# Kernel optimization log

Measured on AMD Instinct MI355X. Metric: run time of the kernel, lower is better.

The kernel has to match this reference:

```python
import jax, jax.numpy as jnp
import numpy as np


def setup_inputs() -> dict:
    key = jax.random.key(0)
    ks = jax.random.split(key, 6)
    N, C, H = 3072, 2048, 16
    hd = C // H  # 128
    x = jax.random.normal(ks[0], (N, C), dtype=jnp.float32)
    # rotary frequencies as cos/sin of per-position angles (real view of complex freqs_cis)
    inv_freq = 1.0 / (10000.0 ** (np.arange(0, hd, 2, dtype=np.float32) / hd))  # [hd/2]
    angles = jnp.arange(N, dtype=jnp.float32)[:, None] * jnp.asarray(inv_freq)[None, :]  # [N, hd/2]
    freqs_cos = jnp.cos(angles)
    freqs_sin = jnp.sin(angles)
    qkv_w = jax.random.normal(ks[1], (3 * C, C), dtype=jnp.float32) * 0.02
    qkv_b = jnp.zeros((3 * C,), dtype=jnp.float32)
    proj_w = jax.random.normal(ks[2], (C, C), dtype=jnp.float32) * 0.02
    proj_b = jnp.zeros((C,), dtype=jnp.float32)
    cu_seqlens = jnp.array([0, 768, 1536, 2304, 3072], dtype=jnp.int32)
    return {
        "x": x, "freqs_cos": freqs_cos, "freqs_sin": freqs_sin,
        "qkv_w": qkv_w, "qkv_b": qkv_b, "proj_w": proj_w, "proj_b": proj_b,
        "cu_seqlens": cu_seqlens, "max_seqlen": 768,
    }


def _rope(t, cos, sin):
    # t: [H, N, hd]; interpret consecutive pairs as complex, multiply by freqs_cis
    tr, ti = t[..., 0::2], t[..., 1::2]              # [H, N, hd/2]
    o_re = tr * cos - ti * sin
    o_im = tr * sin + ti * cos
    return jnp.stack([o_re, o_im], axis=-1).reshape(t.shape)


def reference(x, freqs_cos, freqs_sin, qkv_w, qkv_b, proj_w, proj_b, cu_seqlens, max_seqlen):
    N, C = x.shape
    hd = freqs_cos.shape[-1] * 2
    H = C // hd
    qkv = (x @ qkv_w.T + qkv_b).reshape(N, 3, H, hd).transpose(1, 2, 0, 3)  # [3, H, N, hd]
    q, k, v = qkv[0], qkv[1], qkv[2]
    q = _rope(q, freqs_cos, freqs_sin)
    k = _rope(k, freqs_cos, freqs_sin)
    # varlen attention: block-diagonal mask from cu_seqlens segment membership
    seg = jnp.searchsorted(cu_seqlens[1:], jnp.arange(N), side="right")  # [N]
    mask = seg[:, None] == seg[None, :]                                  # [N, N]
    scale = 1.0 / np.sqrt(hd).astype(np.float32)
    scores = jnp.einsum("hnd,hmd->hnm", q, k) * scale                    # [H, N, N]
    scores = jnp.where(mask[None], scores, jnp.finfo(scores.dtype).min)
    probs = jax.nn.softmax(scores, axis=-1)
    out = jnp.einsum("hnm,hmd->hnd", probs, v)                           # [H, N, hd]
    out = out.transpose(1, 0, 2).reshape(N, C)
    return out @ proj_w.T + proj_b
```

## Files before the change

kernel.cpp:

```cpp
#include <hip/hip_runtime.h>
#include <stdint.h>

#define N_TOK  3072
#define C_DIM  2048
#define K3C    6144
#define NHEAD  16
#define HD     128
#define SEGLEN 768

typedef __attribute__((ext_vector_type(8))) short  short8;
typedef __attribute__((ext_vector_type(4))) float  f32x4;

__device__ __forceinline__ unsigned short f2bf(float f) {
  unsigned u = __builtin_bit_cast(unsigned, f);
  u += 0x7FFFu + ((u >> 16) & 1u);
  return (unsigned short)(u >> 16);
}
__device__ __forceinline__ float bf2f(unsigned short h) {
  unsigned u = ((unsigned)h) << 16;
  return __builtin_bit_cast(float, u);
}
__device__ __forceinline__ void gload_lds16(const void* g, void* l) {
  __builtin_amdgcn_global_load_lds(
      (const __attribute__((address_space(1))) unsigned int*)g,
      (__attribute__((address_space(3))) unsigned int*)l, 16, 0, 0);
}

#define XB_ELEMS    (3072L*2048L)
#define WQKV_ELEMS  (6144L*2048L)
#define WPROJ_ELEMS (2048L*2048L)
__global__ __launch_bounds__(256) void cast_bf16_kernel(
    const float* __restrict__ x, const float* __restrict__ wqkv,
    const float* __restrict__ wproj, unsigned short* __restrict__ xb,
    unsigned short* __restrict__ wqkvb, unsigned short* __restrict__ wprojb) {
  long t = (long)blockIdx.x * 256 + threadIdx.x;
  long i = t * 8;
  const float* src; unsigned short* dst; long off;
  if (i < XB_ELEMS)                   { src = x;     dst = xb;     off = i; }
  else if (i < XB_ELEMS + WQKV_ELEMS) { src = wqkv;  dst = wqkvb;  off = i - XB_ELEMS; }
  else                                { src = wproj; dst = wprojb; off = i - XB_ELEMS - WQKV_ELEMS; }
  f32x4 a = *(const f32x4*)(src + off);
  f32x4 b = *(const f32x4*)(src + off + 4);
  short8 o;
  #pragma unroll
  for (int k = 0; k < 4; ++k) { o[k] = (short)f2bf(a[k]); o[k+4] = (short)f2bf(b[k]); }
  *(short8*)(dst + off) = o;
}

template<bool OUTF32>
__global__ __launch_bounds__(256) void gemm_bt(
    const unsigned short* __restrict__ A, const unsigned short* __restrict__ B,
    const float* __restrict__ bias, void* __restrict__ Cout,
    int M, int N, int K) {
  __shared__ unsigned short sA[128*32];
  __shared__ unsigned short sB[128*32];
  const int tid = threadIdx.x;
  const int w  = tid >> 6, l = tid & 63;
  const int lr = l & 15,  lh = l >> 4;
  const int wr = w >> 1,  wc = w & 1;
  const long row0 = (long)blockIdx.y * 128;
  const long col0 = (long)blockIdx.x * 128;
  f32x4 acc[4][4] = {};

  const int c0 = w*128 + l;
  const int c1 = c0 + 64;
  const int r0 = c0 >> 2, k0 = (c0 & 3) * 8;
  const int r1 = c1 >> 2, k1 = (c1 & 3) * 8;

  for (int kt = 0; kt < K; kt += 32) {
    __syncthreads();
    gload_lds16(A + (row0 + r0)*K + kt + k0, (char*)sA + (size_t)(w*2+0)*1024);
    gload_lds16(A + (row0 + r1)*K + kt + k1, (char*)sA + (size_t)(w*2+1)*1024);
    gload_lds16(B + (col0 + r0)*K + kt + k0, (char*)sB + (size_t)(w*2+0)*1024);
    gload_lds16(B + (col0 + r1)*K + kt + k1, (char*)sB + (size_t)(w*2+1)*1024);
    __syncthreads();

    short8 af[4], bfr[4];
    #pragma unroll
    for (int m = 0; m < 4; ++m) af[m]  = *(const short8*)&sA[(wr*64 + m*16 + lr)*32 + lh*8];
    #pragma unroll
    for (int n = 0; n < 4; ++n) bfr[n] = *(const short8*)&sB[(wc*64 + n*16 + lr)*32 + lh*8];
    #pragma unroll
    for (int m = 0; m < 4; ++m)
      #pragma unroll
      for (int n = 0; n < 4; ++n)
        acc[m][n] = __builtin_amdgcn_mfma_f32_16x16x32_bf16(af[m], bfr[n], acc[m][n], 0, 0, 0);
  }

  #pragma unroll
  for (int n = 0; n < 4; ++n) {
    const long col = col0 + wc*64 + n*16 + lr;
    const float bv = bias[col];
    #pragma unroll
    for (int m = 0; m < 4; ++m) {
      const long rbase = row0 + wr*64 + m*16 + lh*4;
      #pragma unroll
      for (int r = 0; r < 4; ++r) {
        float val = acc[m][n][r] + bv;
        if constexpr (OUTF32) ((float*)Cout)[(rbase + r)*N + col] = val;
        else ((unsigned short*)Cout)[(rbase + r)*N + col] = f2bf(val);
      }
    }
  }
}

__global__ __launch_bounds__(256) void rope_kernel(
    unsigned short* __restrict__ qkv, const float* __restrict__ fcos,
    const float* __restrict__ fsin) {
  long t = (long)blockIdx.x * 256 + threadIdx.x;
  int n  = (int)(t >> 9);
  int col = (int)(t & 511) * 8;
  int j0 = (col & 127) >> 1;
  unsigned short* p = qkv + (long)n * K3C + col;
  short8 v = *(short8*)p;
  f32x4 vc = *(const f32x4*)(fcos + n*64 + j0);
  f32x4 vs = *(const f32x4*)(fsin + n*64 + j0);
  short8 o;
  #pragma unroll
  for (int i = 0; i < 4; ++i) {
    float re = bf2f((unsigned short)v[2*i]);
    float im = bf2f((unsigned short)v[2*i+1]);
    float c = vc[i], s = vs[i];
    o[2*i]   = (short)f2bf(re*c - im*s);
    o[2*i+1] = (short)f2bf(re*s + im*c);
  }
  *(short8*)p = o;
}

__global__ __launch_bounds__(256) void transpose_v_kernel(
    const unsigned short* __restrict__ qkv, unsigned short* __restrict__ vT) {
  __shared__ unsigned short sT[64*64];
  int bidx = blockIdx.x;
  const int nb = (bidx % 48) * 64; bidx /= 48;
  const int db = (bidx & 1) * 64;  bidx >>= 1;
  const int h  = bidx;
  const int tid = threadIdx.x;
  #pragma unroll
  for (int p = 0; p < 2; ++p) {
    int ch = tid + p*256;
    int row = ch >> 3, c8 = ch & 7;
    f32x4 val = *(const f32x4*)(qkv + (long)(nb + row)*K3C + 4096 + h*HD + db + c8*8);
    int off = (row*128 + c8*16) ^ ((row & 7) << 4);
    *(f32x4*)((char*)sT + off) = val;
  }
  __syncthreads();
  #pragma unroll
  for (int p = 0; p < 2; ++p) {
    int ch = tid + p*256;
    int drow = ch >> 3, nc = ch & 7;
    short8 tv;
    #pragma unroll
    for (int j = 0; j < 8; ++j) {
      int nn = nc*8 + j;
      int off = (nn*128 + drow*2) ^ ((nn & 7) << 4);
      tv[j] = *(const short*)((const char*)sT + off);
    }
    *(short8*)(vT + ((long)h*HD + db + drow)*N_TOK + nb + nc*8) = tv;
  }
}

__global__ __launch_bounds__(256) void attn_kernel(
    const unsigned short* __restrict__ qkv, const unsigned short* __restrict__ vT,
    unsigned short* __restrict__ attb) {
  __shared__ unsigned short sK [64*128];
  __shared__ unsigned short sVT[128*64];
  __shared__ unsigned short sP [4][16*72];
  const int tid = threadIdx.x;
  const int w = tid >> 6, l = tid & 63, lr = l & 15, lh = l >> 4;
  int bidx = blockIdx.x;
  const int qt = bidx % 12; bidx /= 12;
  const int h  = bidx & 15; bidx >>= 4;
  const int s  = bidx;
  const int n0 = s*SEGLEN + qt*64;
  const float scale = 0.08838834764831845f;
  const float LOG2E = 1.4426950408889634f;

  short8 aq[4];
  {
    const unsigned short* qrow = qkv + (long)(n0 + w*16 + lr)*K3C + h*HD;
    #pragma unroll
    for (int c = 0; c < 4; ++c) aq[c] = *(const short8*)(qrow + c*32 + lh*8);
  }
  f32x4 o[8] = {};
  float m_r[4] = {-1e30f, -1e30f, -1e30f, -1e30f};
  float l_r[4] = {0.f, 0.f, 0.f, 0.f};

  for (int kt = 0; kt < 12; ++kt) {
    const int kb = s*SEGLEN + kt*64;
    __syncthreads();
    #pragma unroll
    for (int p = 0; p < 4; ++p) {
      int ch = (p*4 + w)*64 + l;
      int key = ch >> 4;
      int kc  = (ch & 15) ^ (key & 7);
      gload_lds16(qkv + (long)(kb + key)*K3C + C_DIM + h*HD + kc*8,
                  (char*)sK + (size_t)(p*4 + w)*1024);
      int d   = ch >> 3;
      int kc2 = (ch & 7) ^ (d & 7);
      gload_lds16(vT + ((long)h*HD + d)*N_TOK + kb + kc2*8,
                  (char*)sVT + (size_t)(p*4 + w)*1024);
    }
    __syncthreads();

    f32x4 sacc[4] = {};
    #pragma unroll
    for (int kd = 0; kd < 4; ++kd)
      #pragma unroll
      for (int kf = 0; kf < 4; ++kf) {
        int key = kf*16 + lr;
        int off = (key*256 + kd*64 + lh*16) ^ ((key & 7) << 4);
        short8 bk = *(const short8*)((const char*)sK + off);
        sacc[kf] = __builtin_amdgcn_mfma_f32_16x16x32_bf16(aq[kd], bk, sacc[kf], 0, 0, 0);
      }

    float alpha[4];
    #pragma unroll
    for (int r = 0; r < 4; ++r) {
      float v0 = fmaxf(fmaxf(sacc[0][r], sacc[1][r]), fmaxf(sacc[2][r], sacc[3][r]));
      #pragma unroll
      for (int sh = 1; sh < 16; sh <<= 1) v0 = fmaxf(v0, __shfl_xor(v0, sh, 64));
      float pm = v0 * scale;
      float mn = fmaxf(m_r[r], pm);
      alpha[r] = __builtin_exp2f((m_r[r] - mn) * LOG2E);
      m_r[r] = mn;
    }
    float rsum[4] = {0.f, 0.f, 0.f, 0.f};
    #pragma unroll
    for (int kf = 0; kf < 4; ++kf)
      #pragma unroll
      for (int r = 0; r < 4; ++r) {
        float pv = __builtin_exp2f((sacc[kf][r]*scale - m_r[r]) * LOG2E);
        rsum[r] += pv;
        sP[w][(lh*4 + r)*72 + kf*16 + lr] = f2bf(pv);
      }
    #pragma unroll
    for (int r = 0; r < 4; ++r) {
      float t = rsum[r];
      #pragma unroll
      for (int sh = 1; sh < 16; sh <<= 1) t += __shfl_xor(t, sh, 64);
      l_r[r] = l_r[r]*alpha[r] + t;
    }
    #pragma unroll
    for (int nf = 0; nf < 8; ++nf)
      #pragma unroll
      for (int r = 0; r < 4; ++r) o[nf][r] *= alpha[r];

    #pragma unroll
    for (int ks = 0; ks < 2; ++ks) {
      short8 ap = *(const short8*)&sP[w][lr*72 + ks*32 + lh*8];
      #pragma unroll
      for (int nf = 0; nf < 8; ++nf) {
        int d = nf*16 + lr;
        int off = (d*128 + ks*64 + lh*16) ^ ((d & 7) << 4);
        short8 bv = *(const short8*)((const char*)sVT + off);
        o[nf] = __builtin_amdgcn_mfma_f32_16x16x32_bf16(ap, bv, o[nf], 0, 0, 0);
      }
    }
  }

  #pragma unroll
  for (int r = 0; r < 4; ++r) {
    float inv = 1.0f / l_r[r];
    int n = n0 + w*16 + lh*4 + r;
    unsigned short* orow = attb + (long)n*C_DIM + h*HD;
    #pragma unroll
    for (int nf = 0; nf < 8; ++nf) orow[nf*16 + lr] = f2bf(o[nf][r] * inv);
  }
}

extern "C" void kernel_launch(void* const* d_in, const int* in_sizes, int n_in,
                              void* d_out, int out_size, void* d_ws, size_t ws_size,
                              hipStream_t stream) {
  (void)in_sizes; (void)n_in; (void)out_size; (void)ws_size;
  const float* x      = (const float*)d_in[0];
  const float* fcos   = (const float*)d_in[1];
  const float* fsin   = (const float*)d_in[2];
  const float* qkv_w  = (const float*)d_in[3];
  const float* qkv_b  = (const float*)d_in[4];
  const float* proj_w = (const float*)d_in[5];
  const float* proj_b = (const float*)d_in[6];

  char* ws = (char*)d_ws;
  unsigned short* xb     = (unsigned short*)(ws + 0L);
  unsigned short* wqkvb  = (unsigned short*)(ws + 12582912L);
  unsigned short* wprojb = (unsigned short*)(ws + 37748736L);
  unsigned short* qkvb   = (unsigned short*)(ws + 46137344L);
  unsigned short* vT     = (unsigned short*)(ws + 83886080L);
  unsigned short* attb   = xb;

  cast_bf16_kernel<<<11264, 256, 0, stream>>>(x, qkv_w, proj_w, xb, wqkvb, wprojb);
  gemm_bt<false><<<dim3(48, 24), 256, 0, stream>>>(xb, wqkvb, qkv_b, qkvb, 3072, 6144, 2048);
  rope_kernel<<<6144, 256, 0, stream>>>(qkvb, fcos, fsin);
  transpose_v_kernel<<<1536, 256, 0, stream>>>(qkvb, vT);
  attn_kernel<<<768, 256, 0, stream>>>(qkvb, vT, attb);
  gemm_bt<true><<<dim3(16, 24), 256, 0, stream>>>(attb, wprojb, proj_b, d_out, 3072, 2048, 2048);
}
```

Before: 419.0 us.

## Replace GEMM with 256x256-tile 8-wave double-buffered pipelined kernel

Replaces the simple 128x128 single-buffered bf16 GEMM with a 512-thread kernel that computes 256x256 output tiles. Global-to-LDS loads are staged ahead into double buffers, with explicit vmcnt waits, barriers and setprio around MFMA bursts, so memory traffic overlaps compute. This raises data reuse per tile and hides load latency. In exchange it uses far more registers and LDS. The projection GEMM now launches only 96 blocks, which may underfill the GPU.

```diff
diff --git a/kernel.cpp b/kernel.cpp
--- a/kernel.cpp
+++ b/kernel.cpp
@@ -47,58 +47,100 @@
   *(short8*)(dst + off) = o;
 }
 
+#define VM4 asm volatile("s_waitcnt vmcnt(4)" ::: "memory");
+#define VM0 asm volatile("s_waitcnt vmcnt(0)" ::: "memory");
+
+#define STAGE(buf, mat, h, t, BASE) do { \
+  const unsigned short* _src = (BASE) + (size_t)(tid & 255) * (size_t)K_ \
+                               + (size_t)((t)*64 + ((h)*4 + (tid >> 8))*8); \
+  char* _l = ldsB + ((((buf)*2 + (mat))*8 + (h)*4) * 4096) + wv*1024; \
+  gload_lds16(_src,      _l); \
+  gload_lds16(_src + 16, _l + 8192); \
+} while (0)
+
+#define PHASE(buf, kk, mh, LOADB, STAGES, WAIT) do { \
+  short8 aF[4]; \
+  _Pragma("unroll") \
+  for (int j = 0; j < 4; ++j) \
+    aF[j] = *(const short8*)&sH[buf][0][(kk)*4 + lh][wr*128 + ((mh)*4 + j)*16 + lr][0]; \
+  if (LOADB) { \
+    _Pragma("unroll") \
+    for (int n = 0; n < 4; ++n) \
+      bF[n] = *(const short8*)&sH[buf][1][(kk)*4 + lh][wc*64 + n*16 + lr][0]; \
+  } \
+  STAGES \
+  __builtin_amdgcn_s_barrier(); \
+  asm volatile("s_waitcnt lgkmcnt(0)" ::: "memory"); \
+  __builtin_amdgcn_sched_barrier(0); \
+  __builtin_amdgcn_s_setprio(1); \
+  _Pragma("unroll") \
+  for (int j = 0; j < 4; ++j) { \
+    _Pragma("unroll") \
+    for (int n = 0; n < 4; ++n) \
+      acc[(mh)*4 + j][n] = __builtin_amdgcn_mfma_f32_16x16x32_bf16(aF[j], bF[n], acc[(mh)*4 + j][n], 0, 0, 0); \
+  } \
+  __builtin_amdgcn_s_setprio(0); \
+  __builtin_amdgcn_sched_barrier(0); \
+  WAIT \
+  __builtin_amdgcn_s_barrier(); \
+} while (0)
+
 template<bool OUTF32>
-__global__ __launch_bounds__(256) void gemm_bt(
+__global__ __launch_bounds__(512, 2) void gemm8p(
     const unsigned short* __restrict__ A, const unsigned short* __restrict__ B,
     const float* __restrict__ bias, void* __restrict__ Cout,
-    int M, int N, int K) {
-  __shared__ unsigned short sA[128*32];
-  __shared__ unsigned short sB[128*32];
+    int N, int K_) {
+  __shared__ __align__(16) unsigned short sH[2][2][8][256][8];
+  char* ldsB = (char*)&sH[0][0][0][0][0];
   const int tid = threadIdx.x;
-  const int w  = tid >> 6, l = tid & 63;
-  const int lr = l & 15,  lh = l >> 4;
-  const int wr = w >> 1,  wc = w & 1;
-  const long row0 = (long)blockIdx.y * 128;
-  const long col0 = (long)blockIdx.x * 128;
-  f32x4 acc[4][4] = {};
-
-  const int c0 = w*128 + l;
-  const int c1 = c0 + 64;
-  const int r0 = c0 >> 2, k0 = (c0 & 3) * 8;
-  const int r1 = c1 >> 2, k1 = (c1 & 3) * 8;
-
-  for (int kt = 0; kt < K; kt += 32) {
-    __syncthreads();
-    gload_lds16(A + (row0 + r0)*K + kt + k0, (char*)sA + (size_t)(w*2+0)*1024);
-    gload_lds16(A + (row0 + r1)*K + kt + k1, (char*)sA + (size_t)(w*2+1)*1024);
-    gload_lds16(B + (col0 + r0)*K + kt + k0, (char*)sB + (size_t)(w*2+0)*1024);
-    gload_lds16(B + (col0 + r1)*K + kt + k1, (char*)sB + (size_t)(w*2+1)*1024);
-    __syncthreads();
-
-    short8 af[4], bfr[4];
-    #pragma unroll
-    for (int m = 0; m < 4; ++m) af[m]  = *(const short8*)&sA[(wr*64 + m*16 + lr)*32 + lh*8];
-    #pragma unroll
-    for (int n = 0; n < 4; ++n) bfr[n] = *(const short8*)&sB[(wc*64 + n*16 + lr)*32 + lh*8];
-    #pragma unroll
-    for (int m = 0; m < 4; ++m)
-      #pragma unroll
-      for (int n = 0; n < 4; ++n)
-        acc[m][n] = __builtin_amdgcn_mfma_f32_16x16x32_bf16(af[m], bfr[n], acc[m][n], 0, 0, 0);
-  }
+  const int wv = tid >> 6, l = tid & 63, lr = l & 15, lh = l >> 4;
+  const int wr = wv >> 2, wc = wv & 3;
+  const long row0 = (long)blockIdx.y * 256;
+  const long col0 = (long)blockIdx.x * 256;
+  const unsigned short* Ab = A + row0 * K_;
+  const unsigned short* Bb = B + col0 * K_;
+  f32x4 acc[8][4] = {};
+  short8 bF[4];
+
+  STAGE(0,0,0, 0, Ab); STAGE(0,1,0, 0, Bb); STAGE(0,0,1, 0, Ab); STAGE(0,1,1, 0, Bb);
+  STAGE(1,0,0, 1, Ab); STAGE(1,1,0, 1, Bb);
+  VM4
+  __builtin_amdgcn_s_barrier();
+
+  const int NITER = K_ >> 7;
+  int t0 = 0;
+  #pragma unroll 1
+  for (int it = 0; it < NITER - 1; ++it, t0 += 2) {
+    PHASE(0,0,0, 1, STAGE(1,0,1, t0+1, Ab);, );
+    PHASE(0,0,1, 0, STAGE(1,1,1, t0+1, Bb);, );
+    PHASE(0,1,0, 1, STAGE(0,0,0, t0+2, Ab);, );
+    PHASE(0,1,1, 0, STAGE(0,1,0, t0+2, Bb);, VM4);
+    PHASE(1,0,0, 1, STAGE(0,0,1, t0+2, Ab);, );
+    PHASE(1,0,1, 0, STAGE(0,1,1, t0+2, Bb);, );
+    PHASE(1,1,0, 1, STAGE(1,0,0, t0+3, Ab);, );
+    PHASE(1,1,1, 0, STAGE(1,1,0, t0+3, Bb);, VM4);
+  }
+  PHASE(0,0,0, 1, STAGE(1,0,1, t0+1, Ab);, );
+  PHASE(0,0,1, 0, STAGE(1,1,1, t0+1, Bb);, );
+  PHASE(0,1,0, 1, , );
+  PHASE(0,1,1, 0, , VM0);
+  PHASE(1,0,0, 1, , );
+  PHASE(1,0,1, 0, , );
+  PHASE(1,1,0, 1, , );
+  PHASE(1,1,1, 0, , );
 
   #pragma unroll
   for (int n = 0; n < 4; ++n) {
     const long col = col0 + wc*64 + n*16 + lr;
     const float bv = bias[col];
     #pragma unroll
-    for (int m = 0; m < 4; ++m) {
-      const long rbase = row0 + wr*64 + m*16 + lh*4;
+    for (int m = 0; m < 8; ++m) {
+      const long rb = row0 + wr*128 + m*16 + lh*4;
       #pragma unroll
       for (int r = 0; r < 4; ++r) {
         float val = acc[m][n][r] + bv;
-        if constexpr (OUTF32) ((float*)Cout)[(rbase + r)*N + col] = val;
-        else ((unsigned short*)Cout)[(rbase + r)*N + col] = f2bf(val);
+        if constexpr (OUTF32) ((float*)Cout)[(rb + r)*N + col] = val;
+        else ((unsigned short*)Cout)[(rb + r)*N + col] = f2bf(val);
       }
     }
   }
@@ -289,9 +331,9 @@
   unsigned short* attb   = xb;
 
   cast_bf16_kernel<<<11264, 256, 0, stream>>>(x, qkv_w, proj_w, xb, wqkvb, wprojb);
-  gemm_bt<false><<<dim3(48, 24), 256, 0, stream>>>(xb, wqkvb, qkv_b, qkvb, 3072, 6144, 2048);
+  gemm8p<false><<<dim3(24, 12), 512, 0, stream>>>(xb, wqkvb, qkv_b, qkvb, 6144, 2048);
   rope_kernel<<<6144, 256, 0, stream>>>(qkvb, fcos, fsin);
   transpose_v_kernel<<<1536, 256, 0, stream>>>(qkvb, vT);
   attn_kernel<<<768, 256, 0, stream>>>(qkvb, vT, attb);
-  gemm_bt<true><<<dim3(16, 24), 256, 0, stream>>>(attb, wprojb, proj_b, d_out, 3072, 2048, 2048);
-}
+  gemm8p<true><<<dim3(8, 12), 512, 0, stream>>>(attb, wprojb, proj_b, d_out, 2048, 2048);
+}
```

Result: slower. 478.4 us (+14.2%).
